# Performance work log

Hardware: AMD Instinct MI355X
Metric: run time of the kernel (lower is better)

The kernel has to match this reference:

```python
import jax, jax.numpy as jnp
import numpy as np

N_NODES = 100000
N_EDGES = 3200000


def gcn_conv(x, edge_index, W, b, n_nodes):
    # PyG GCNConv default: add self-loops, symmetric degree normalization,
    # linear transform, scatter-add aggregation at target nodes, add bias.
    src = jnp.concatenate([edge_index[0], jnp.arange(n_nodes, dtype=edge_index.dtype)])
    dst = jnp.concatenate([edge_index[1], jnp.arange(n_nodes, dtype=edge_index.dtype)])
    deg = jax.ops.segment_sum(jnp.ones_like(dst, dtype=x.dtype), dst, num_segments=n_nodes)
    dinv = jnp.where(deg > 0, jax.lax.rsqrt(jnp.maximum(deg, 1e-12)), 0.0)
    norm = dinv[src] * dinv[dst]            # [E+N]
    h = x @ W                               # [N, F_out]
    msg = h[src] * norm[:, None]            # gather + scale
    out = jax.ops.segment_sum(msg, dst, num_segments=n_nodes)
    return out + b


def setup_inputs() -> dict:
    key = jax.random.key(0)
    k1, k2, k3, k4 = jax.random.split(key, 4)
    x = jax.random.normal(k1, (N_NODES, 2), dtype=jnp.float32)
    edge_index = jax.random.randint(k2, (2, N_EDGES), 0, N_NODES, dtype=jnp.int64)
    # Glorot-ish init for weights, zero bias (PyG default zeros bias).
    W1 = jax.random.normal(k3, (2, 16), dtype=jnp.float32) * (1.0 / np.sqrt(2.0))
    b1 = jnp.zeros((16,), dtype=jnp.float32)
    W2 = jax.random.normal(k4, (16, 2), dtype=jnp.float32) * (1.0 / np.sqrt(16.0))
    b2 = jnp.zeros((2,), dtype=jnp.float32)
    return {"x": x, "edge_index": edge_index, "W1": W1, "b1": b1, "W2": W2, "b2": b2}


def reference(x, edge_index, W1, b1, W2, b2):
    n = x.shape[0]
    h = gcn_conv(x, edge_index, W1, b1, n)
    h = jax.nn.relu(h)
    h = gcn_conv(h, edge_index, W2, b2, n)
    return jax.nn.log_softmax(h, axis=1)
```

## Files before the change

kernel.cpp:

```cpp
#include <hip/hip_runtime.h>
#include <math.h>


#define BLK 256
#define NTILE 512
#define EPTMAX 6400
#define MAXB 512
#define MSK 0x1FFFFu
#define SRTMAX 10240


__global__ void k_hist(const int* __restrict__ dst, int* __restrict__ table,
                       int e, int ept, int nbkt) {
    __shared__ int h[MAXB];
    int tile = blockIdx.x;
    for (int i = threadIdx.x; i < MAXB; i += BLK) h[i] = 0;
    __syncthreads();
    int lo = tile * ept;
    int hi = min(lo + ept, e);
    for (int i = lo + 4 * threadIdx.x; i < hi; i += 4 * BLK) {
        int4 d4 = *(const int4*)(dst + i);
        atomicAdd(&h[d4.x >> 8], 1);
        atomicAdd(&h[d4.y >> 8], 1);
        atomicAdd(&h[d4.z >> 8], 1);
        atomicAdd(&h[d4.w >> 8], 1);
    }
    __syncthreads();
    for (int i = threadIdx.x; i < nbkt; i += BLK)
        table[tile * nbkt + i] = h[i];
}

__global__ void k_scan_col(int* __restrict__ table, int* __restrict__ tot, int nbkt) {
    __shared__ int wsum[NTILE / 64];
    int b = blockIdx.x;
    int t = threadIdx.x;
    int v = table[t * nbkt + b];
    int x = v;
    int lane = t & 63;
#pragma unroll
    for (int ofs = 1; ofs < 64; ofs <<= 1) {
        int y = __shfl_up(x, ofs, 64);
        if (lane >= ofs) x += y;
    }
    if (lane == 63) wsum[t >> 6] = x;
    __syncthreads();
    if (t < NTILE / 64) {
        int s = wsum[t];
        int w = s;
#pragma unroll
        for (int ofs = 1; ofs < NTILE / 64; ofs <<= 1) {
            int y = __shfl_up(w, ofs, 64);
            if (t >= ofs) w += y;
        }
        wsum[t] = w - s;
    }
    __syncthreads();
    int incl = x + wsum[t >> 6];
    table[t * nbkt + b] = incl - v;
    if (t == NTILE - 1) tot[b] = incl;
}

__global__ void k_scan_tot(const int* __restrict__ tot, int* __restrict__ bkt_off, int nbkt) {
    __shared__ int wsum[MAXB / 64];
    int t = threadIdx.x;
    int v = (t < nbkt) ? tot[t] : 0;
    int x = v;
    int lane = t & 63;
#pragma unroll
    for (int ofs = 1; ofs < 64; ofs <<= 1) {
        int y = __shfl_up(x, ofs, 64);
        if (lane >= ofs) x += y;
    }
    if (lane == 63) wsum[t >> 6] = x;
    __syncthreads();
    if (t < MAXB / 64) {
        int s = wsum[t];
        int w = s;
#pragma unroll
        for (int ofs = 1; ofs < MAXB / 64; ofs <<= 1) {
            int y = __shfl_up(w, ofs, 64);
            if (t >= ofs) w += y;
        }
        wsum[t] = w - s;
    }
    __syncthreads();
    int incl = x + wsum[t >> 6];
    if (t < nbkt) bkt_off[t] = incl - v;
    if (t == nbkt - 1) bkt_off[nbkt] = incl;
}

__global__ void k_scatter(const int* __restrict__ src, const int* __restrict__ dst,
                          const int* __restrict__ table, const int* __restrict__ tot,
                          const int* __restrict__ bkt_off, unsigned* __restrict__ sorted,
                          int e, int ept, int nbkt) {
    __shared__ int cur[MAXB];
    __shared__ int base2[MAXB];
    __shared__ unsigned stage[EPTMAX];
    __shared__ unsigned short stage_b[EPTMAX];
    __shared__ int wpart[BLK / 64];
    int tile = blockIdx.x;
    int t = threadIdx.x;
    int lo = tile * ept;
    int hi = min(lo + ept, e);
    int total = hi - lo;

    int b0 = 2 * t, b1 = 2 * t + 1;
    int c0 = 0, c1 = 0, g0 = 0, g1 = 0;
    if (b0 < nbkt) {
        int base = table[tile * nbkt + b0];
        int next = (tile < NTILE - 1) ? table[(tile + 1) * nbkt + b0] : tot[b0];
        c0 = next - base;
        g0 = bkt_off[b0] + base;
    }
    if (b1 < nbkt) {
        int base = table[tile * nbkt + b1];
        int next = (tile < NTILE - 1) ? table[(tile + 1) * nbkt + b1] : tot[b1];
        c1 = next - base;
        g1 = bkt_off[b1] + base;
    }
    int p = c0 + c1;
    int x = p;
    int lane = t & 63;
#pragma unroll
    for (int ofs = 1; ofs < 64; ofs <<= 1) {
        int y = __shfl_up(x, ofs, 64);
        if (lane >= ofs) x += y;
    }
    if (lane == 63) wpart[t >> 6] = x;
    __syncthreads();
    if (t < BLK / 64) {
        int s = wpart[t];
        int w = s;
#pragma unroll
        for (int ofs = 1; ofs < BLK / 64; ofs <<= 1) {
            int y = __shfl_up(w, ofs, 64);
            if (t >= ofs) w += y;
        }
        wpart[t] = w - s;
    }
    __syncthreads();
    int E = x + wpart[t >> 6] - p;
    cur[b0] = E;
    cur[b1] = E + c0;
    if (b0 < nbkt) base2[b0] = g0 - E;
    if (b1 < nbkt) base2[b1] = g1 - (E + c0);
    __syncthreads();

    for (int i = lo + 4 * t; i < hi; i += 4 * BLK) {
        int4 s4 = *(const int4*)(src + i);
        int4 d4 = *(const int4*)(dst + i);
        int b, pos;
        b = d4.x >> 8; pos = atomicAdd(&cur[b], 1);
        stage[pos] = (unsigned)s4.x | ((unsigned)(d4.x & 255) << 17); stage_b[pos] = (unsigned short)b;
        b = d4.y >> 8; pos = atomicAdd(&cur[b], 1);
        stage[pos] = (unsigned)s4.y | ((unsigned)(d4.y & 255) << 17); stage_b[pos] = (unsigned short)b;
        b = d4.z >> 8; pos = atomicAdd(&cur[b], 1);
        stage[pos] = (unsigned)s4.z | ((unsigned)(d4.z & 255) << 17); stage_b[pos] = (unsigned short)b;
        b = d4.w >> 8; pos = atomicAdd(&cur[b], 1);
        stage[pos] = (unsigned)s4.w | ((unsigned)(d4.w & 255) << 17); stage_b[pos] = (unsigned short)b;
    }
    __syncthreads();
    for (int j = t; j < total; j += BLK) {
        int b = stage_b[j];
        sorted[base2[b] + j] = stage[j];
    }
}

__global__ __launch_bounds__(256) void k_cnt(
        const unsigned* __restrict__ sorted, const int* __restrict__ bkt_off,
        const float* __restrict__ x, float* __restrict__ dinv,
        float* __restrict__ xp, int* __restrict__ nodeoff, int n, int nbkt) {
    __shared__ int cnt[256];
    __shared__ int wsum[4];
    int b = blockIdx.x, t = threadIdx.x;
    cnt[t] = 0;
    __syncthreads();
    int lo = bkt_off[b], hi = bkt_off[b + 1];
    int la = lo & ~3;
    for (int i = la + 4 * t; i < hi; i += 4 * 256) {
        uint4 r = *(const uint4*)(sorted + i);
        if (i >= lo && i + 4 <= hi) {
            atomicAdd(&cnt[r.x >> 17], 1);
            atomicAdd(&cnt[r.y >> 17], 1);
            atomicAdd(&cnt[r.z >> 17], 1);
            atomicAdd(&cnt[r.w >> 17], 1);
        } else {
            if (i + 0 >= lo && i + 0 < hi) atomicAdd(&cnt[r.x >> 17], 1);
            if (i + 1 >= lo && i + 1 < hi) atomicAdd(&cnt[r.y >> 17], 1);
            if (i + 2 >= lo && i + 2 < hi) atomicAdd(&cnt[r.z >> 17], 1);
            if (i + 3 >= lo && i + 3 < hi) atomicAdd(&cnt[r.w >> 17], 1);
        }
    }
    __syncthreads();
    int c = cnt[t];
    int node = (b << 8) + t;
    if (node < n) {
        float d = rsqrtf((float)c + 1.0f);
        dinv[node] = d;
        float2 xv = ((const float2*)x)[node];
        ((float2*)xp)[node] = make_float2(d * xv.x, d * xv.y);
    }
    int xsc = c;
    int lane = t & 63;
#pragma unroll
    for (int ofs = 1; ofs < 64; ofs <<= 1) {
        int y = __shfl_up(xsc, ofs, 64);
        if (lane >= ofs) xsc += y;
    }
    if (lane == 63) wsum[t >> 6] = xsc;
    __syncthreads();
    if (t < 4) {
        int s = wsum[t];
        int w = s;
#pragma unroll
        for (int ofs = 1; ofs < 4; ofs <<= 1) {
            int y = __shfl_up(w, ofs, 64);
            if (t >= ofs) w += y;
        }
        wsum[t] = w - s;
    }
    __syncthreads();
    int excl = xsc + wsum[t >> 6] - c;
    nodeoff[node] = lo + excl;
    if (b == nbkt - 1 && t == 255) nodeoff[node + 1] = hi;
}

__global__ __launch_bounds__(1024) void k_sagg1(
        const unsigned* __restrict__ sorted, const int* __restrict__ bkt_off,
        const int* __restrict__ nodeoff, const float* __restrict__ xp,
        const float* __restrict__ dinv, const float* __restrict__ W1,
        const float* __restrict__ b1, const float* __restrict__ W2,
        float* __restrict__ gp, int n) {
    __shared__ unsigned srt[SRTMAX];
    __shared__ int cur[256];
    __shared__ int stt[257];
    int b = blockIdx.x, t = threadIdx.x;
    int lo = bkt_off[b], hi = bkt_off[b + 1];
    if (t < 256) {
        int s = nodeoff[(b << 8) + t] - lo;
        cur[t] = s;
        stt[t] = s;
        if (t == 255) stt[256] = hi - lo;
    }
    __syncthreads();
    int la = lo & ~3;
    for (int i = la + 4 * t; i < hi; i += 4 * 1024) {
        uint4 r = *(const uint4*)(sorted + i);
        if (i >= lo && i + 4 <= hi) {
            int p0 = atomicAdd(&cur[r.x >> 17], 1); srt[p0] = r.x & MSK;
            int p1 = atomicAdd(&cur[r.y >> 17], 1); srt[p1] = r.y & MSK;
            int p2 = atomicAdd(&cur[r.z >> 17], 1); srt[p2] = r.z & MSK;
            int p3 = atomicAdd(&cur[r.w >> 17], 1); srt[p3] = r.w & MSK;
        } else {
            if (i + 0 >= lo && i + 0 < hi) { int p0 = atomicAdd(&cur[r.x >> 17], 1); srt[p0] = r.x & MSK; }
            if (i + 1 >= lo && i + 1 < hi) { int p1 = atomicAdd(&cur[r.y >> 17], 1); srt[p1] = r.y & MSK; }
            if (i + 2 >= lo && i + 2 < hi) { int p2 = atomicAdd(&cur[r.z >> 17], 1); srt[p2] = r.z & MSK; }
            if (i + 3 >= lo && i + 3 < hi) { int p3 = atomicAdd(&cur[r.w >> 17], 1); srt[p3] = r.w & MSK; }
        }
    }
    __syncthreads();

    int nl = t >> 2, q = t & 3;
    int gid = (b << 8) + nl;
    int s = stt[nl], epos = stt[nl + 1];
    const float2* xp2 = (const float2*)xp;
    float sx = 0.f, sy = 0.f;
    for (int p = s + q; p < epos; p += 4) {
        float2 f = xp2[srt[p]];
        sx += f.x; sy += f.y;
    }
    sx += __shfl_xor(sx, 1); sy += __shfl_xor(sy, 1);
    sx += __shfl_xor(sx, 2); sy += __shfl_xor(sy, 2);
    if (q == 0 && gid < n) {
        float d = dinv[gid];
        float2 xv = xp2[gid];
        float ax = d * (sx + xv.x), ay = d * (sy + xv.y);
        float g0 = 0.f, g1 = 0.f;
#pragma unroll
        for (int f = 0; f < 16; ++f) {
            float h = fmaf(ax, W1[f], fmaf(ay, W1[16 + f], b1[f]));
            h = fmaxf(h, 0.0f);
            g0 = fmaf(h, W2[2 * f + 0], g0);
            g1 = fmaf(h, W2[2 * f + 1], g1);
        }
        ((float2*)gp)[gid] = make_float2(d * g0, d * g1);
    }
}

__global__ __launch_bounds__(1024) void k_sagg2(
        const unsigned* __restrict__ sorted, const int* __restrict__ bkt_off,
        const int* __restrict__ nodeoff, const float* __restrict__ gp,
        const float* __restrict__ dinv, const float* __restrict__ b2,
        float* __restrict__ out, int n) {
    __shared__ unsigned srt[SRTMAX];
    __shared__ int cur[256];
    __shared__ int stt[257];
    int b = blockIdx.x, t = threadIdx.x;
    int lo = bkt_off[b], hi = bkt_off[b + 1];
    if (t < 256) {
        int s = nodeoff[(b << 8) + t] - lo;
        cur[t] = s;
        stt[t] = s;
        if (t == 255) stt[256] = hi - lo;
    }
    __syncthreads();
    int la = lo & ~3;
    for (int i = la + 4 * t; i < hi; i += 4 * 1024) {
        uint4 r = *(const uint4*)(sorted + i);
        if (i >= lo && i + 4 <= hi) {
            int p0 = atomicAdd(&cur[r.x >> 17], 1); srt[p0] = r.x & MSK;
            int p1 = atomicAdd(&cur[r.y >> 17], 1); srt[p1] = r.y & MSK;
            int p2 = atomicAdd(&cur[r.z >> 17], 1); srt[p2] = r.z & MSK;
            int p3 = atomicAdd(&cur[r.w >> 17], 1); srt[p3] = r.w & MSK;
        } else {
            if (i + 0 >= lo && i + 0 < hi) { int p0 = atomicAdd(&cur[r.x >> 17], 1); srt[p0] = r.x & MSK; }
            if (i + 1 >= lo && i + 1 < hi) { int p1 = atomicAdd(&cur[r.y >> 17], 1); srt[p1] = r.y & MSK; }
            if (i + 2 >= lo && i + 2 < hi) { int p2 = atomicAdd(&cur[r.z >> 17], 1); srt[p2] = r.z & MSK; }
            if (i + 3 >= lo && i + 3 < hi) { int p3 = atomicAdd(&cur[r.w >> 17], 1); srt[p3] = r.w & MSK; }
        }
    }
    __syncthreads();

    int nl = t >> 2, q = t & 3;
    int gid = (b << 8) + nl;
    int s = stt[nl], epos = stt[nl + 1];
    const float2* gp2 = (const float2*)gp;
    float sx = 0.f, sy = 0.f;
    for (int p = s + q; p < epos; p += 4) {
        float2 f = gp2[srt[p]];
        sx += f.x; sy += f.y;
    }
    sx += __shfl_xor(sx, 1); sy += __shfl_xor(sy, 1);
    sx += __shfl_xor(sx, 2); sy += __shfl_xor(sy, 2);
    if (q == 0 && gid < n) {
        float d = dinv[gid];
        float2 gv = gp2[gid];
        float z0 = d * (sx + gv.x) + b2[0];
        float z1 = d * (sy + gv.y) + b2[1];
        float m = fmaxf(z0, z1);
        float lse = m + logf(expf(z0 - m) + expf(z1 - m));
        ((float2*)out)[gid] = make_float2(z0 - lse, z1 - lse);
    }
}

extern "C" void kernel_launch(void* const* d_in, const int* in_sizes, int n_in,
                              void* d_out, int out_size, void* d_ws, size_t ws_size,
                              hipStream_t stream) {
    const float* x  = (const float*)d_in[0];
    const int*   ei = (const int*)d_in[1];
    const float* W1 = (const float*)d_in[2];
    const float* b1 = (const float*)d_in[3];
    const float* W2 = (const float*)d_in[4];
    const float* b2 = (const float*)d_in[5];
    float* out = (float*)d_out;

    const int n = in_sizes[0] / 2;
    const int e = in_sizes[1] / 2;
    const int* src = ei;
    const int* dst = ei + e;

    const int nbkt = (n + 255) >> 8;
    int ept = (((e + NTILE - 1) / NTILE) + 3) & ~3;

    char* base = (char*)d_ws;
    size_t off = 0;
    auto take = [&](size_t bytes) { char* p = base + off; off += (bytes + 255) & ~(size_t)255; return p; };
    unsigned* sorted  = (unsigned*)take(((size_t)e + 8) * 4);
    int*      table   = (int*)take((size_t)NTILE * nbkt * 4);
    int*      tot     = (int*)take((size_t)MAXB * 4);
    int*      bkt_off = (int*)take((size_t)(MAXB + 1) * 4);
    int*      nodeoff = (int*)take((size_t)(nbkt * 256 + 64) * 4);
    float*    dinv    = (float*)take((size_t)n * 4);
    float*    xp      = (float*)take((size_t)n * 8);
    float*    gp      = (float*)take((size_t)n * 8);

    k_hist    <<<NTILE, BLK, 0, stream>>>(dst, table, e, ept, nbkt);
    k_scan_col<<<nbkt, NTILE, 0, stream>>>(table, tot, nbkt);
    k_scan_tot<<<1, MAXB, 0, stream>>>(tot, bkt_off, nbkt);
    k_scatter <<<NTILE, BLK, 0, stream>>>(src, dst, table, tot, bkt_off, sorted, e, ept, nbkt);
    k_cnt     <<<nbkt, 256, 0, stream>>>(sorted, bkt_off, x, dinv, xp, nodeoff, n, nbkt);
    k_sagg1   <<<nbkt, 1024, 0, stream>>>(sorted, bkt_off, nodeoff, xp, dinv, W1, b1, W2, gp, n);
    k_sagg2   <<<nbkt, 1024, 0, stream>>>(sorted, bkt_off, nodeoff, gp, dinv, b2, out, n);
}
```

Baseline: 142.0 us.

## Fuse both GCN aggregation layers into one cooperative kernel with grid sync

Merges the two per-bucket aggregation kernels into a single cooperative launch that builds the LDS-sorted neighbour list once, computes layer-1 output, does a grid-wide sync, then aggregates layer 2 from the same LDS list. This removes one kernel launch and the second pass that re-reads and re-sorts the bucketed edge list. If the cooperative launch fails (for example when too many blocks are needed to be co-resident), it falls back to the original two kernels. Needing every block resident at once can limit occupancy, and the grid sync adds a global barrier.

```diff
diff --git a/kernel.cpp b/kernel.cpp
--- a/kernel.cpp
+++ b/kernel.cpp
@@ -1,5 +1,8 @@
 #include <hip/hip_runtime.h>
+#include <hip/hip_cooperative_groups.h>
 #include <math.h>
+
+namespace cg = cooperative_groups;
 
 
 #define BLK 256
@@ -224,6 +227,92 @@
     nodeoff[node] = lo + excl;
     if (b == nbkt - 1 && t == 255) nodeoff[node + 1] = hi;
 }
+
+__global__ __launch_bounds__(1024) void k_sagg12(
+        const unsigned* __restrict__ sorted, const int* __restrict__ bkt_off,
+        const int* __restrict__ nodeoff, const float* __restrict__ xp,
+        const float* __restrict__ dinv,
+        const float* __restrict__ W1, const float* __restrict__ b1,
+        const float* __restrict__ W2, const float* __restrict__ b2,
+        float* __restrict__ gp, float* __restrict__ out, int n) {
+    __shared__ unsigned srt[SRTMAX];
+    __shared__ int cur[256];
+    __shared__ int stt[257];
+    cg::grid_group grid = cg::this_grid();
+    int b = blockIdx.x, t = threadIdx.x;
+    int lo = bkt_off[b], hi = bkt_off[b + 1];
+    if (t < 256) {
+        int s = nodeoff[(b << 8) + t] - lo;
+        cur[t] = s;
+        stt[t] = s;
+        if (t == 255) stt[256] = hi - lo;
+    }
+    __syncthreads();
+    int la = lo & ~3;
+    for (int i = la + 4 * t; i < hi; i += 4 * 1024) {
+        uint4 r = *(const uint4*)(sorted + i);
+        if (i >= lo && i + 4 <= hi) {
+            int p0 = atomicAdd(&cur[r.x >> 17], 1); srt[p0] = r.x & MSK;
+            int p1 = atomicAdd(&cur[r.y >> 17], 1); srt[p1] = r.y & MSK;
+            int p2 = atomicAdd(&cur[r.z >> 17], 1); srt[p2] = r.z & MSK;
+            int p3 = atomicAdd(&cur[r.w >> 17], 1); srt[p3] = r.w & MSK;
+        } else {
+            if (i + 0 >= lo && i + 0 < hi) { int p0 = atomicAdd(&cur[r.x >> 17], 1); srt[p0] = r.x & MSK; }
+            if (i + 1 >= lo && i + 1 < hi) { int p1 = atomicAdd(&cur[r.y >> 17], 1); srt[p1] = r.y & MSK; }
+            if (i + 2 >= lo && i + 2 < hi) { int p2 = atomicAdd(&cur[r.z >> 17], 1); srt[p2] = r.z & MSK; }
+            if (i + 3 >= lo && i + 3 < hi) { int p3 = atomicAdd(&cur[r.w >> 17], 1); srt[p3] = r.w & MSK; }
+        }
+    }
+    __syncthreads();
+
+    int nl = t >> 2, q = t & 3;
+    int gid = (b << 8) + nl;
+    int s0 = stt[nl], e0 = stt[nl + 1];
+    const float2* xp2 = (const float2*)xp;
+    float sx = 0.f, sy = 0.f;
+    for (int p = s0 + q; p < e0; p += 4) {
+        float2 f = xp2[srt[p]];
+        sx += f.x; sy += f.y;
+    }
+    sx += __shfl_xor(sx, 1); sy += __shfl_xor(sy, 1);
+    sx += __shfl_xor(sx, 2); sy += __shfl_xor(sy, 2);
+    if (q == 0 && gid < n) {
+        float d = dinv[gid];
+        float2 xv = xp2[gid];
+        float ax = d * (sx + xv.x), ay = d * (sy + xv.y);
+        float g0 = 0.f, g1 = 0.f;
+#pragma unroll
+        for (int f = 0; f < 16; ++f) {
+            float h = fmaf(ax, W1[f], fmaf(ay, W1[16 + f], b1[f]));
+            h = fmaxf(h, 0.0f);
+            g0 = fmaf(h, W2[2 * f + 0], g0);
+            g1 = fmaf(h, W2[2 * f + 1], g1);
+        }
+        ((float2*)gp)[gid] = make_float2(d * g0, d * g1);
+    }
+
+    __threadfence();
+    grid.sync();
+
+    const float2* gp2 = (const float2*)gp;
+    float tx = 0.f, ty = 0.f;
+    for (int p = s0 + q; p < e0; p += 4) {
+        float2 f = gp2[srt[p]];
+        tx += f.x; ty += f.y;
+    }
+    tx += __shfl_xor(tx, 1); ty += __shfl_xor(ty, 1);
+    tx += __shfl_xor(tx, 2); ty += __shfl_xor(ty, 2);
+    if (q == 0 && gid < n) {
+        float d = dinv[gid];
+        float2 gv = gp2[gid];
+        float z0 = d * (tx + gv.x) + b2[0];
+        float z1 = d * (ty + gv.y) + b2[1];
+        float m = fmaxf(z0, z1);
+        float lse = m + logf(expf(z0 - m) + expf(z1 - m));
+        ((float2*)out)[gid] = make_float2(z0 - lse, z1 - lse);
+    }
+}
+
 
 __global__ __launch_bounds__(1024) void k_sagg1(
         const unsigned* __restrict__ sorted, const int* __restrict__ bkt_off,
@@ -259,7 +348,6 @@
         }
     }
     __syncthreads();
-
     int nl = t >> 2, q = t & 3;
     int gid = (b << 8) + nl;
     int s = stt[nl], epos = stt[nl + 1];
@@ -320,7 +408,6 @@
         }
     }
     __syncthreads();
-
     int nl = t >> 2, q = t & 3;
     int gid = (b << 8) + nl;
     int s = stt[nl], epos = stt[nl + 1];
@@ -379,6 +466,16 @@
     k_scan_tot<<<1, MAXB, 0, stream>>>(tot, bkt_off, nbkt);
     k_scatter <<<NTILE, BLK, 0, stream>>>(src, dst, table, tot, bkt_off, sorted, e, ept, nbkt);
     k_cnt     <<<nbkt, 256, 0, stream>>>(sorted, bkt_off, x, dinv, xp, nodeoff, n, nbkt);
-    k_sagg1   <<<nbkt, 1024, 0, stream>>>(sorted, bkt_off, nodeoff, xp, dinv, W1, b1, W2, gp, n);
-    k_sagg2   <<<nbkt, 1024, 0, stream>>>(sorted, bkt_off, nodeoff, gp, dinv, b2, out, n);
-}
+
+    int nn = n;
+    void* args[] = {(void*)&sorted, (void*)&bkt_off, (void*)&nodeoff, (void*)&xp,
+                    (void*)&dinv, (void*)&W1, (void*)&b1, (void*)&W2, (void*)&b2,
+                    (void*)&gp, (void*)&out, (void*)&nn};
+    hipError_t cerr = hipLaunchCooperativeKernel((const void*)k_sagg12, dim3(nbkt), dim3(1024),
+                                                 args, 0, stream);
+    if (cerr != hipSuccess) {
+        (void)hipGetLastError();
+        k_sagg1<<<nbkt, 1024, 0, stream>>>(sorted, bkt_off, nodeoff, xp, dinv, W1, b1, W2, gp, n);
+        k_sagg2<<<nbkt, 1024, 0, stream>>>(sorted, bkt_off, nodeoff, gp, dinv, b2, out, n);
+    }
+}
```

New measurement: 318.3 us. 124% more time.

## Replace histogram and scan bucketing with single-pass atomic fixed-stride bucket scatter

Applied to the files above, without the earlier changes.

Drops the three-kernel histogram, column-scan and total-scan pipeline. Each tile now builds a local histogram in shared memory, then reserves space in each bucket with a global atomicAdd on a per-bucket cursor. Buckets sit at a fixed stride of BSTRIDE slots, so no global prefix sum is needed and the downstream kernels read bucket bounds straight from the cursor counts. The dst column is staged in LDS so it is read from global memory only once. In exchange, edge order within a bucket becomes nondeterministic, and the code assumes no bucket holds more than BSTRIDE edges, an assumption already made by SRTMAX.

```diff
diff --git a/kernel.cpp b/kernel.cpp
--- a/kernel.cpp
+++ b/kernel.cpp
@@ -8,95 +8,18 @@
 #define MAXB 512
 #define MSK 0x1FFFFu
 #define SRTMAX 10240
-
-
-__global__ void k_hist(const int* __restrict__ dst, int* __restrict__ table,
-                       int e, int ept, int nbkt) {
-    __shared__ int h[MAXB];
-    int tile = blockIdx.x;
-    for (int i = threadIdx.x; i < MAXB; i += BLK) h[i] = 0;
-    __syncthreads();
-    int lo = tile * ept;
-    int hi = min(lo + ept, e);
-    for (int i = lo + 4 * threadIdx.x; i < hi; i += 4 * BLK) {
-        int4 d4 = *(const int4*)(dst + i);
-        atomicAdd(&h[d4.x >> 8], 1);
-        atomicAdd(&h[d4.y >> 8], 1);
-        atomicAdd(&h[d4.z >> 8], 1);
-        atomicAdd(&h[d4.w >> 8], 1);
-    }
-    __syncthreads();
-    for (int i = threadIdx.x; i < nbkt; i += BLK)
-        table[tile * nbkt + i] = h[i];
-}
-
-__global__ void k_scan_col(int* __restrict__ table, int* __restrict__ tot, int nbkt) {
-    __shared__ int wsum[NTILE / 64];
-    int b = blockIdx.x;
-    int t = threadIdx.x;
-    int v = table[t * nbkt + b];
-    int x = v;
-    int lane = t & 63;
-#pragma unroll
-    for (int ofs = 1; ofs < 64; ofs <<= 1) {
-        int y = __shfl_up(x, ofs, 64);
-        if (lane >= ofs) x += y;
-    }
-    if (lane == 63) wsum[t >> 6] = x;
-    __syncthreads();
-    if (t < NTILE / 64) {
-        int s = wsum[t];
-        int w = s;
-#pragma unroll
-        for (int ofs = 1; ofs < NTILE / 64; ofs <<= 1) {
-            int y = __shfl_up(w, ofs, 64);
-            if (t >= ofs) w += y;
-        }
-        wsum[t] = w - s;
-    }
-    __syncthreads();
-    int incl = x + wsum[t >> 6];
-    table[t * nbkt + b] = incl - v;
-    if (t == NTILE - 1) tot[b] = incl;
-}
-
-__global__ void k_scan_tot(const int* __restrict__ tot, int* __restrict__ bkt_off, int nbkt) {
-    __shared__ int wsum[MAXB / 64];
-    int t = threadIdx.x;
-    int v = (t < nbkt) ? tot[t] : 0;
-    int x = v;
-    int lane = t & 63;
-#pragma unroll
-    for (int ofs = 1; ofs < 64; ofs <<= 1) {
-        int y = __shfl_up(x, ofs, 64);
-        if (lane >= ofs) x += y;
-    }
-    if (lane == 63) wsum[t >> 6] = x;
-    __syncthreads();
-    if (t < MAXB / 64) {
-        int s = wsum[t];
-        int w = s;
-#pragma unroll
-        for (int ofs = 1; ofs < MAXB / 64; ofs <<= 1) {
-            int y = __shfl_up(w, ofs, 64);
-            if (t >= ofs) w += y;
-        }
-        wsum[t] = w - s;
-    }
-    __syncthreads();
-    int incl = x + wsum[t >> 6];
-    if (t < nbkt) bkt_off[t] = incl - v;
-    if (t == nbkt - 1) bkt_off[nbkt] = incl;
-}
-
-__global__ void k_scatter(const int* __restrict__ src, const int* __restrict__ dst,
-                          const int* __restrict__ table, const int* __restrict__ tot,
-                          const int* __restrict__ bkt_off, unsigned* __restrict__ sorted,
-                          int e, int ept, int nbkt) {
+#define BSTRIDE 10240
+
+__global__ __launch_bounds__(256) void k_scatter2(
+        const int* __restrict__ src, const int* __restrict__ dst,
+        int* __restrict__ gcur, unsigned* __restrict__ sorted,
+        int e, int ept, int nbkt) {
+    __shared__ int hcnt[MAXB];
     __shared__ int cur[MAXB];
     __shared__ int base2[MAXB];
     __shared__ unsigned stage[EPTMAX];
     __shared__ unsigned short stage_b[EPTMAX];
+    __shared__ unsigned ldst[EPTMAX];
     __shared__ int wpart[BLK / 64];
     int tile = blockIdx.x;
     int t = threadIdx.x;
@@ -104,20 +27,25 @@
     int hi = min(lo + ept, e);
     int total = hi - lo;
 
+    for (int i = t; i < MAXB; i += BLK) hcnt[i] = 0;
+    __syncthreads();
+
+    for (int i = lo + 4 * t; i < hi; i += 4 * BLK) {
+        int4 d4 = *(const int4*)(dst + i);
+        int j = i - lo;
+        ldst[j + 0] = (unsigned)d4.x;
+        ldst[j + 1] = (unsigned)d4.y;
+        ldst[j + 2] = (unsigned)d4.z;
+        ldst[j + 3] = (unsigned)d4.w;
+        atomicAdd(&hcnt[d4.x >> 8], 1);
+        atomicAdd(&hcnt[d4.y >> 8], 1);
+        atomicAdd(&hcnt[d4.z >> 8], 1);
+        atomicAdd(&hcnt[d4.w >> 8], 1);
+    }
+    __syncthreads();
+
     int b0 = 2 * t, b1 = 2 * t + 1;
-    int c0 = 0, c1 = 0, g0 = 0, g1 = 0;
-    if (b0 < nbkt) {
-        int base = table[tile * nbkt + b0];
-        int next = (tile < NTILE - 1) ? table[(tile + 1) * nbkt + b0] : tot[b0];
-        c0 = next - base;
-        g0 = bkt_off[b0] + base;
-    }
-    if (b1 < nbkt) {
-        int base = table[tile * nbkt + b1];
-        int next = (tile < NTILE - 1) ? table[(tile + 1) * nbkt + b1] : tot[b1];
-        c1 = next - base;
-        g1 = bkt_off[b1] + base;
-    }
+    int c0 = hcnt[b0], c1 = hcnt[b1];
     int p = c0 + c1;
     int x = p;
     int lane = t & 63;
@@ -142,22 +70,26 @@
     int E = x + wpart[t >> 6] - p;
     cur[b0] = E;
     cur[b1] = E + c0;
-    if (b0 < nbkt) base2[b0] = g0 - E;
-    if (b1 < nbkt) base2[b1] = g1 - (E + c0);
+    int g0 = 0, g1 = 0;
+    if (b0 < nbkt && c0 > 0) g0 = atomicAdd(&gcur[b0], c0);
+    if (b1 < nbkt && c1 > 0) g1 = atomicAdd(&gcur[b1], c1);
+    base2[b0] = b0 * BSTRIDE + g0 - E;
+    base2[b1] = b1 * BSTRIDE + g1 - (E + c0);
     __syncthreads();
 
     for (int i = lo + 4 * t; i < hi; i += 4 * BLK) {
         int4 s4 = *(const int4*)(src + i);
-        int4 d4 = *(const int4*)(dst + i);
+        int j = i - lo;
+        unsigned d0 = ldst[j + 0], d1 = ldst[j + 1], d2 = ldst[j + 2], d3 = ldst[j + 3];
         int b, pos;
-        b = d4.x >> 8; pos = atomicAdd(&cur[b], 1);
-        stage[pos] = (unsigned)s4.x | ((unsigned)(d4.x & 255) << 17); stage_b[pos] = (unsigned short)b;
-        b = d4.y >> 8; pos = atomicAdd(&cur[b], 1);
-        stage[pos] = (unsigned)s4.y | ((unsigned)(d4.y & 255) << 17); stage_b[pos] = (unsigned short)b;
-        b = d4.z >> 8; pos = atomicAdd(&cur[b], 1);
-        stage[pos] = (unsigned)s4.z | ((unsigned)(d4.z & 255) << 17); stage_b[pos] = (unsigned short)b;
-        b = d4.w >> 8; pos = atomicAdd(&cur[b], 1);
-        stage[pos] = (unsigned)s4.w | ((unsigned)(d4.w & 255) << 17); stage_b[pos] = (unsigned short)b;
+        b = (int)(d0 >> 8); pos = atomicAdd(&cur[b], 1);
+        stage[pos] = (unsigned)s4.x | ((d0 & 255u) << 17); stage_b[pos] = (unsigned short)b;
+        b = (int)(d1 >> 8); pos = atomicAdd(&cur[b], 1);
+        stage[pos] = (unsigned)s4.y | ((d1 & 255u) << 17); stage_b[pos] = (unsigned short)b;
+        b = (int)(d2 >> 8); pos = atomicAdd(&cur[b], 1);
+        stage[pos] = (unsigned)s4.z | ((d2 & 255u) << 17); stage_b[pos] = (unsigned short)b;
+        b = (int)(d3 >> 8); pos = atomicAdd(&cur[b], 1);
+        stage[pos] = (unsigned)s4.w | ((d3 & 255u) << 17); stage_b[pos] = (unsigned short)b;
     }
     __syncthreads();
     for (int j = t; j < total; j += BLK) {
@@ -167,28 +99,28 @@
 }
 
 __global__ __launch_bounds__(256) void k_cnt(
-        const unsigned* __restrict__ sorted, const int* __restrict__ bkt_off,
+        const unsigned* __restrict__ sorted, const int* __restrict__ bcnt,
         const float* __restrict__ x, float* __restrict__ dinv,
-        float* __restrict__ xp, int* __restrict__ nodeoff, int n, int nbkt) {
+        float* __restrict__ xp, int* __restrict__ nodeoff, int n) {
     __shared__ int cnt[256];
     __shared__ int wsum[4];
     int b = blockIdx.x, t = threadIdx.x;
     cnt[t] = 0;
     __syncthreads();
-    int lo = bkt_off[b], hi = bkt_off[b + 1];
-    int la = lo & ~3;
-    for (int i = la + 4 * t; i < hi; i += 4 * 256) {
+    int lo = b * BSTRIDE;
+    int hi = lo + bcnt[b];
+    for (int i = lo + 4 * t; i < hi; i += 4 * 256) {
         uint4 r = *(const uint4*)(sorted + i);
-        if (i >= lo && i + 4 <= hi) {
+        if (i + 4 <= hi) {
             atomicAdd(&cnt[r.x >> 17], 1);
             atomicAdd(&cnt[r.y >> 17], 1);
             atomicAdd(&cnt[r.z >> 17], 1);
             atomicAdd(&cnt[r.w >> 17], 1);
         } else {
-            if (i + 0 >= lo && i + 0 < hi) atomicAdd(&cnt[r.x >> 17], 1);
-            if (i + 1 >= lo && i + 1 < hi) atomicAdd(&cnt[r.y >> 17], 1);
-            if (i + 2 >= lo && i + 2 < hi) atomicAdd(&cnt[r.z >> 17], 1);
-            if (i + 3 >= lo && i + 3 < hi) atomicAdd(&cnt[r.w >> 17], 1);
+            if (i + 0 < hi) atomicAdd(&cnt[r.x >> 17], 1);
+            if (i + 1 < hi) atomicAdd(&cnt[r.y >> 17], 1);
+            if (i + 2 < hi) atomicAdd(&cnt[r.z >> 17], 1);
+            if (i + 3 < hi) atomicAdd(&cnt[r.w >> 17], 1);
         }
     }
     __syncthreads();
@@ -222,11 +154,10 @@
     __syncthreads();
     int excl = xsc + wsum[t >> 6] - c;
     nodeoff[node] = lo + excl;
-    if (b == nbkt - 1 && t == 255) nodeoff[node + 1] = hi;
 }
 
 __global__ __launch_bounds__(1024) void k_sagg1(
-        const unsigned* __restrict__ sorted, const int* __restrict__ bkt_off,
+        const unsigned* __restrict__ sorted, const int* __restrict__ bcnt,
         const int* __restrict__ nodeoff, const float* __restrict__ xp,
         const float* __restrict__ dinv, const float* __restrict__ W1,
         const float* __restrict__ b1, const float* __restrict__ W2,
@@ -235,7 +166,8 @@
     __shared__ int cur[256];
     __shared__ int stt[257];
     int b = blockIdx.x, t = threadIdx.x;
-    int lo = bkt_off[b], hi = bkt_off[b + 1];
+    int lo = b * BSTRIDE;
+    int hi = lo + bcnt[b];
     if (t < 256) {
         int s = nodeoff[(b << 8) + t] - lo;
         cur[t] = s;
@@ -243,19 +175,18 @@
         if (t == 255) stt[256] = hi - lo;
     }
     __syncthreads();
-    int la = lo & ~3;
-    for (int i = la + 4 * t; i < hi; i += 4 * 1024) {
+    for (int i = lo + 4 * t; i < hi; i += 4 * 1024) {
         uint4 r = *(const uint4*)(sorted + i);
-        if (i >= lo && i + 4 <= hi) {
+        if (i + 4 <= hi) {
             int p0 = atomicAdd(&cur[r.x >> 17], 1); srt[p0] = r.x & MSK;
             int p1 = atomicAdd(&cur[r.y >> 17], 1); srt[p1] = r.y & MSK;
             int p2 = atomicAdd(&cur[r.z >> 17], 1); srt[p2] = r.z & MSK;
             int p3 = atomicAdd(&cur[r.w >> 17], 1); srt[p3] = r.w & MSK;
         } else {
-            if (i + 0 >= lo && i + 0 < hi) { int p0 = atomicAdd(&cur[r.x >> 17], 1); srt[p0] = r.x & MSK; }
-            if (i + 1 >= lo && i + 1 < hi) { int p1 = atomicAdd(&cur[r.y >> 17], 1); srt[p1] = r.y & MSK; }
-            if (i + 2 >= lo && i + 2 < hi) { int p2 = atomicAdd(&cur[r.z >> 17], 1); srt[p2] = r.z & MSK; }
-            if (i + 3 >= lo && i + 3 < hi) { int p3 = atomicAdd(&cur[r.w >> 17], 1); srt[p3] = r.w & MSK; }
+            if (i + 0 < hi) { int p0 = atomicAdd(&cur[r.x >> 17], 1); srt[p0] = r.x & MSK; }
+            if (i + 1 < hi) { int p1 = atomicAdd(&cur[r.y >> 17], 1); srt[p1] = r.y & MSK; }
+            if (i + 2 < hi) { int p2 = atomicAdd(&cur[r.z >> 17], 1); srt[p2] = r.z & MSK; }
+            if (i + 3 < hi) { int p3 = atomicAdd(&cur[r.w >> 17], 1); srt[p3] = r.w & MSK; }
         }
     }
     __syncthreads();
@@ -288,7 +219,7 @@
 }
 
 __global__ __launch_bounds__(1024) void k_sagg2(
-        const unsigned* __restrict__ sorted, const int* __restrict__ bkt_off,
+        const unsigned* __restrict__ sorted, const int* __restrict__ bcnt,
         const int* __restrict__ nodeoff, const float* __restrict__ gp,
         const float* __restrict__ dinv, const float* __restrict__ b2,
         float* __restrict__ out, int n) {
@@ -296,7 +227,8 @@
     __shared__ int cur[256];
     __shared__ int stt[257];
     int b = blockIdx.x, t = threadIdx.x;
-    int lo = bkt_off[b], hi = bkt_off[b + 1];
+    int lo = b * BSTRIDE;
+    int hi = lo + bcnt[b];
     if (t < 256) {
         int s = nodeoff[(b << 8) + t] - lo;
         cur[t] = s;
@@ -304,19 +236,18 @@
         if (t == 255) stt[256] = hi - lo;
     }
     __syncthreads();
-    int la = lo & ~3;
-    for (int i = la + 4 * t; i < hi; i += 4 * 1024) {
+    for (int i = lo + 4 * t; i < hi; i += 4 * 1024) {
         uint4 r = *(const uint4*)(sorted + i);
-        if (i >= lo && i + 4 <= hi) {
+        if (i + 4 <= hi) {
             int p0 = atomicAdd(&cur[r.x >> 17], 1); srt[p0] = r.x & MSK;
             int p1 = atomicAdd(&cur[r.y >> 17], 1); srt[p1] = r.y & MSK;
             int p2 = atomicAdd(&cur[r.z >> 17], 1); srt[p2] = r.z & MSK;
             int p3 = atomicAdd(&cur[r.w >> 17], 1); srt[p3] = r.w & MSK;
         } else {
-            if (i + 0 >= lo && i + 0 < hi) { int p0 = atomicAdd(&cur[r.x >> 17], 1); srt[p0] = r.x & MSK; }
-            if (i + 1 >= lo && i + 1 < hi) { int p1 = atomicAdd(&cur[r.y >> 17], 1); srt[p1] = r.y & MSK; }
-            if (i + 2 >= lo && i + 2 < hi) { int p2 = atomicAdd(&cur[r.z >> 17], 1); srt[p2] = r.z & MSK; }
-            if (i + 3 >= lo && i + 3 < hi) { int p3 = atomicAdd(&cur[r.w >> 17], 1); srt[p3] = r.w & MSK; }
+            if (i + 0 < hi) { int p0 = atomicAdd(&cur[r.x >> 17], 1); srt[p0] = r.x & MSK; }
+            if (i + 1 < hi) { int p1 = atomicAdd(&cur[r.y >> 17], 1); srt[p1] = r.y & MSK; }
+            if (i + 2 < hi) { int p2 = atomicAdd(&cur[r.z >> 17], 1); srt[p2] = r.z & MSK; }
+            if (i + 3 < hi) { int p3 = atomicAdd(&cur[r.w >> 17], 1); srt[p3] = r.w & MSK; }
         }
     }
     __syncthreads();
@@ -365,20 +296,16 @@
     char* base = (char*)d_ws;
     size_t off = 0;
     auto take = [&](size_t bytes) { char* p = base + off; off += (bytes + 255) & ~(size_t)255; return p; };
-    unsigned* sorted  = (unsigned*)take(((size_t)e + 8) * 4);
-    int*      table   = (int*)take((size_t)NTILE * nbkt * 4);
-    int*      tot     = (int*)take((size_t)MAXB * 4);
-    int*      bkt_off = (int*)take((size_t)(MAXB + 1) * 4);
+    unsigned* sorted  = (unsigned*)take(((size_t)nbkt * BSTRIDE + 8) * 4);
+    int*      gcur    = (int*)take((size_t)MAXB * 4);
     int*      nodeoff = (int*)take((size_t)(nbkt * 256 + 64) * 4);
     float*    dinv    = (float*)take((size_t)n * 4);
     float*    xp      = (float*)take((size_t)n * 8);
     float*    gp      = (float*)take((size_t)n * 8);
 
-    k_hist    <<<NTILE, BLK, 0, stream>>>(dst, table, e, ept, nbkt);
-    k_scan_col<<<nbkt, NTILE, 0, stream>>>(table, tot, nbkt);
-    k_scan_tot<<<1, MAXB, 0, stream>>>(tot, bkt_off, nbkt);
-    k_scatter <<<NTILE, BLK, 0, stream>>>(src, dst, table, tot, bkt_off, sorted, e, ept, nbkt);
-    k_cnt     <<<nbkt, 256, 0, stream>>>(sorted, bkt_off, x, dinv, xp, nodeoff, n, nbkt);
-    k_sagg1   <<<nbkt, 1024, 0, stream>>>(sorted, bkt_off, nodeoff, xp, dinv, W1, b1, W2, gp, n);
-    k_sagg2   <<<nbkt, 1024, 0, stream>>>(sorted, bkt_off, nodeoff, gp, dinv, b2, out, n);
-}
+    hipMemsetAsync(gcur, 0, (size_t)MAXB * 4, stream);
+    k_scatter2<<<NTILE, BLK, 0, stream>>>(src, dst, gcur, sorted, e, ept, nbkt);
+    k_cnt     <<<nbkt, 256, 0, stream>>>(sorted, gcur, x, dinv, xp, nodeoff, n);
+    k_sagg1   <<<nbkt, 1024, 0, stream>>>(sorted, gcur, nodeoff, xp, dinv, W1, b1, W2, gp, n);
+    k_sagg2   <<<nbkt, 1024, 0, stream>>>(sorted, gcur, nodeoff, gp, dinv, b2, out, n);
+}
```

Result: slower. 152.4 us (+7.3%).
